# Kernel optimization log

Measured on AMD Instinct MI355X. Metric: run time of the kernel, lower is better.

The kernel has to match this reference:

```python
import jax, jax.numpy as jnp
import numpy as np

H, W = 14, 14
HEAD_DIM = 32
HEADS = 24
HIDDEN = 768
RATE = 0.2
EPS = 1e-5


def _bias_idxs(h, w):
    # map_bias indexing: for flat pair index x over (h*w)^2
    x = jnp.arange(h * h * w * w)
    m, n = x // (h * w), x % (h * w)
    i, j = m // w, m % w
    ip, jp = n // w, n % w
    return (i - ip + h) * (2 * w) + (j - jp + w)


def _layer_norm(x, g, b):
    mu = jnp.mean(x, axis=-1, keepdims=True)
    var = jnp.mean(jnp.square(x - mu), axis=-1, keepdims=True)
    return (x - mu) * jax.lax.rsqrt(var + EPS) * g + b


def setup_inputs() -> dict:
    key = jax.random.key(0)
    ks = jax.random.split(key, 10)
    N, L = 64, H * W
    s = lambda fan_in: 1.0 / np.sqrt(fan_in)
    return {
        "x": jax.random.normal(ks[0], (N, L, HIDDEN), jnp.float32),
        "rel_bias": jax.random.uniform(ks[1], (1, 2 * H * 2 * W), jnp.float32, -0.5, 0.5),
        "wq": jax.random.normal(ks[2], (HEAD_DIM, HEAD_DIM), jnp.float32) * s(HEAD_DIM),
        "wk": jax.random.normal(ks[3], (HEAD_DIM, HEAD_DIM), jnp.float32) * s(HEAD_DIM),
        "wv": jax.random.normal(ks[4], (HEAD_DIM, HEAD_DIM), jnp.float32) * s(HEAD_DIM),
        "w_out": jax.random.normal(ks[5], (HIDDEN, HIDDEN), jnp.float32) * s(HIDDEN),
        "ln1_g": jnp.ones((HIDDEN,), jnp.float32),
        "ln1_b": jnp.zeros((HIDDEN,), jnp.float32),
        "ln2_g": jnp.ones((HIDDEN,), jnp.float32),
        "ln2_b": jnp.zeros((HIDDEN,), jnp.float32),
        "w1": jax.random.normal(ks[6], (4 * HIDDEN, HIDDEN), jnp.float32) * s(HIDDEN),
        "b1": jnp.zeros((4 * HIDDEN,), jnp.float32),
        "w2": jax.random.normal(ks[7], (HIDDEN, 4 * HIDDEN), jnp.float32) * s(4 * HIDDEN),
        "b2": jnp.zeros((HIDDEN,), jnp.float32),
    }


def reference(x, rel_bias, wq, wk, wv, w_out, ln1_g, ln1_b, ln2_g, ln2_b, w1, b1, w2, b2):
    N, L, _ = x.shape

    def attn(m):
        xh = m.reshape(N, L, HEADS, HEAD_DIM)
        # Linear(head_dim, head_dim) shared across heads; torch Linear: y = x @ W^T
        q = jnp.einsum("nlhd,ed->nlhe", xh, wq)
        k = jnp.einsum("nlhd,ed->nlhe", xh, wk)
        v = jnp.einsum("nlhd,ed->nlhe", xh, wv)
        scores = jnp.einsum("nqhd,nkhd->nhqk", q, k)
        bias = rel_bias[0][_bias_idxs(H, W)].reshape(1, 1, L, L)
        a = jax.nn.softmax((scores + bias) / np.sqrt(HEAD_DIM), axis=-1)
        o = jnp.einsum("nhqk,nkhd->nqhd", a, v).reshape(N, L, HIDDEN)
        return o @ w_out.T

    def ffn(m):
        h = jax.nn.gelu(m @ w1.T + b1, approximate=False)
        return h @ w2.T + b2

    # training-mode stochastic depth: deterministic scaling by RATE
    x = (x + attn(_layer_norm(x, ln1_g, ln1_b))) * RATE
    x = (x + ffn(_layer_norm(x, ln2_g, ln2_b))) * RATE
    return x
```

## Files before the change

### kernel.cpp

```cpp
#include <hip/hip_runtime.h>
#include <math.h>

#define NB    64
#define LSEQ  196
#define HID   768
#define NHEAD 24
#define HDIM  32
#define FFN   3072
#define ROWS  (NB * LSEQ)
#define RATE  0.2f
#define LN_EPS 1e-5f

typedef unsigned short bf16_t;
typedef short s16x8 __attribute__((ext_vector_type(8)));
typedef float f32x4 __attribute__((ext_vector_type(4)));

__device__ __forceinline__ unsigned short f2bf(float f) {
    unsigned u = __float_as_uint(f);
    unsigned r = u + 0x7fffu + ((u >> 16) & 1u);
    return (unsigned short)(r >> 16);
}

#define GLOAD_LDS16(g, l)                                                  \
    __builtin_amdgcn_global_load_lds(                                      \
        (const __attribute__((address_space(1))) void*)(g),                \
        (__attribute__((address_space(3))) void*)(l), 16, 0, 0)

#define WOUT4 (HID * HID / 4)
#define W14   (FFN * HID / 4)
__global__ __launch_bounds__(256) void cvt_w_kernel(
    const float* __restrict__ w_out, const float* __restrict__ w1,
    const float* __restrict__ w2, bf16_t* __restrict__ wob,
    bf16_t* __restrict__ w1b, bf16_t* __restrict__ w2b)
{
    int i = blockIdx.x * 256 + threadIdx.x;
    const float* src; bf16_t* dst; int off;
    if (i < WOUT4)            { src = w_out; dst = wob; off = i; }
    else if (i < WOUT4 + W14) { src = w1;    dst = w1b; off = i - WOUT4; }
    else                      { src = w2;    dst = w2b; off = i - WOUT4 - W14; }
    float4 v = ((const float4*)src)[off];
    uint2 p;
    p.x = (unsigned)f2bf(v.x) | ((unsigned)f2bf(v.y) << 16);
    p.y = (unsigned)f2bf(v.z) | ((unsigned)f2bf(v.w) << 16);
    ((uint2*)dst)[off] = p;
}

__global__ __launch_bounds__(256) void ln_kernel(
    const float* __restrict__ x, const float* __restrict__ g,
    const float* __restrict__ b, bf16_t* __restrict__ yv)
{
    int row = blockIdx.x;
    int tid = threadIdx.x;
    const float* xr = x + (size_t)row * HID;
    float v0 = xr[tid], v1 = xr[tid + 256], v2 = xr[tid + 512];
    __shared__ float rs[256], rs2[256];
    rs[tid]  = v0 + v1 + v2;
    rs2[tid] = v0 * v0 + v1 * v1 + v2 * v2;
    __syncthreads();
    for (int off = 128; off > 0; off >>= 1) {
        if (tid < off) { rs[tid] += rs[tid + off]; rs2[tid] += rs2[tid + off]; }
        __syncthreads();
    }
    float mean = rs[0] * (1.0f / HID);
    float var  = rs2[0] * (1.0f / HID) - mean * mean;
    float rstd = rsqrtf(var + LN_EPS);
    bf16_t* yr = yv + (size_t)row * HID;
    yr[tid]       = f2bf((v0 - mean) * rstd * g[tid]       + b[tid]);
    yr[tid + 256] = f2bf((v1 - mean) * rstd * g[tid + 256] + b[tid + 256]);
    yr[tid + 512] = f2bf((v2 - mean) * rstd * g[tid + 512] + b[tid + 512]);
}

#define QKV_T 16
__global__ __launch_bounds__(256) void ln_qkv_mfma_kernel(
    const float* __restrict__ x, const float* __restrict__ g,
    const float* __restrict__ b,
    const float* __restrict__ wq, const float* __restrict__ wk,
    const float* __restrict__ wv,
    bf16_t* __restrict__ q, bf16_t* __restrict__ k, bf16_t* __restrict__ v)
{
    int tid = threadIdx.x;
    int w = tid >> 6, lane = tid & 63;
    int lr = lane & 15, lq = lane >> 4;

    __shared__ __align__(16) bf16_t Xs[QKV_T * 24 * 32];
    __shared__ __align__(16) bf16_t Wqs[32 * 32];
    __shared__ __align__(16) bf16_t Wks[32 * 32];
    __shared__ __align__(16) bf16_t Wvs[32 * 32];

    for (int i = tid; i < 1024; i += 256) {
        Wqs[i] = f2bf(wq[i]);
        Wks[i] = f2bf(wk[i]);
        Wvs[i] = f2bf(wv[i]);
    }

    float4 gv[3], bv[3];
#pragma unroll
    for (int i = 0; i < 3; i++) {
        gv[i] = ((const float4*)g)[lane + i * 64];
        bv[i] = ((const float4*)b)[lane + i * 64];
    }

    for (int j = 0; j < 4; j++) {
        int lt = w * 4 + j;
        size_t row = (size_t)blockIdx.x * QKV_T + lt;
        const float4* xr = (const float4*)(x + row * HID);
        float4 xv[3];
        float s = 0.f, s2 = 0.f;
#pragma unroll
        for (int i = 0; i < 3; i++) {
            xv[i] = xr[lane + i * 64];
            s  += xv[i].x + xv[i].y + xv[i].z + xv[i].w;
            s2 += xv[i].x * xv[i].x + xv[i].y * xv[i].y
                + xv[i].z * xv[i].z + xv[i].w * xv[i].w;
        }
#pragma unroll
        for (int d = 1; d < 64; d <<= 1) {
            s  += __shfl_xor(s, d);
            s2 += __shfl_xor(s2, d);
        }
        float mean = s * (1.0f / HID);
        float rstd = rsqrtf(s2 * (1.0f / HID) - mean * mean + LN_EPS);
#pragma unroll
        for (int i = 0; i < 3; i++) {
            int idx  = (lane + i * 64) * 4;
            int head = idx >> 5, d0 = idx & 31;
            float o0 = (xv[i].x - mean) * rstd * gv[i].x + bv[i].x;
            float o1 = (xv[i].y - mean) * rstd * gv[i].y + bv[i].y;
            float o2 = (xv[i].z - mean) * rstd * gv[i].z + bv[i].z;
            float o3 = (xv[i].w - mean) * rstd * gv[i].w + bv[i].w;
            uint2 p;
            p.x = (unsigned)f2bf(o0) | ((unsigned)f2bf(o1) << 16);
            p.y = (unsigned)f2bf(o2) | ((unsigned)f2bf(o3) << 16);
            *(uint2*)&Xs[(lt * 24 + head) * 32 + d0] = p;
        }
    }
    __syncthreads();

    s16x8 bq[2], bk[2], bvv[2];
    bq[0]  = *(const s16x8*)&Wqs[lr * 32 + lq * 8];
    bq[1]  = *(const s16x8*)&Wqs[(16 + lr) * 32 + lq * 8];
    bk[0]  = *(const s16x8*)&Wks[lr * 32 + lq * 8];
    bk[1]  = *(const s16x8*)&Wks[(16 + lr) * 32 + lq * 8];
    bvv[0] = *(const s16x8*)&Wvs[lr * 32 + lq * 8];
    bvv[1] = *(const s16x8*)&Wvs[(16 + lr) * 32 + lq * 8];

    for (int t = 0; t < 6; t++) {
        int tile = w * 6 + t;
        s16x8 aX = *(const s16x8*)&Xs[(tile * 16 + lr) * 32 + lq * 8];
        f32x4 z = {};
        f32x4 aq0 = __builtin_amdgcn_mfma_f32_16x16x32_bf16(aX, bq[0],  z, 0, 0, 0);
        f32x4 aq1 = __builtin_amdgcn_mfma_f32_16x16x32_bf16(aX, bq[1],  z, 0, 0, 0);
        f32x4 ak0 = __builtin_amdgcn_mfma_f32_16x16x32_bf16(aX, bk[0],  z, 0, 0, 0);
        f32x4 ak1 = __builtin_amdgcn_mfma_f32_16x16x32_bf16(aX, bk[1],  z, 0, 0, 0);
        f32x4 av0 = __builtin_amdgcn_mfma_f32_16x16x32_bf16(aX, bvv[0], z, 0, 0, 0);
        f32x4 av1 = __builtin_amdgcn_mfma_f32_16x16x32_bf16(aX, bvv[1], z, 0, 0, 0);
        int rbase = tile * 16 + lq * 4;
#pragma unroll
        for (int r = 0; r < 4; r++) {
            int xrow = rbase + r;
            int t_loc = xrow / 24, head = xrow - t_loc * 24;
            size_t gb = ((size_t)blockIdx.x * QKV_T + t_loc) * HID + head * 32;
            q[gb + lr]      = f2bf(aq0[r]);
            q[gb + 16 + lr] = f2bf(aq1[r]);
            k[gb + lr]      = f2bf(ak0[r]);
            k[gb + 16 + lr] = f2bf(ak1[r]);
            v[gb + lr]      = f2bf(av0[r]);
            v[gb + 16 + lr] = f2bf(av1[r]);
        }
    }
}

#define VT_S 232
#define P_S  40

__global__ __launch_bounds__(256) void attn_mfma_kernel(
    const bf16_t* __restrict__ q, const bf16_t* __restrict__ k,
    const bf16_t* __restrict__ v, const float* __restrict__ rel_bias,
    bf16_t* __restrict__ o)
{
    int h = blockIdx.x;
    int n = blockIdx.y;
    int tid = threadIdx.x;
    int w = tid >> 6, lane = tid & 63;
    int lr = lane & 15;
    int lq = lane >> 4;

    __shared__ __align__(16) bf16_t Qs[208 * 32];
    __shared__ __align__(16) bf16_t Ks[224 * 32];
    __shared__ __align__(16) bf16_t Vt[32 * VT_S];
    __shared__ float bsh[28 * 28];
    __shared__ __align__(16) bf16_t Ps[4][16 * P_S];

    size_t base = (size_t)n * LSEQ * HID + (size_t)h * HDIM;

    for (int i = tid; i < 224 * 4; i += 256) {
        int r = i >> 2, c = i & 3;
        uint4 kv = make_uint4(0, 0, 0, 0);
        if (r < 196) kv = *(const uint4*)&k[base + (size_t)r * HID + c * 8];
        *(uint4*)&Ks[r * 32 + c * 8] = kv;
        if (r < 208) {
            uint4 qv = make_uint4(0, 0, 0, 0);
            if (r < 196) qv = *(const uint4*)&q[base + (size_t)r * HID + c * 8];
            *(uint4*)&Qs[r * 32 + c * 8] = qv;
        }
    }
    for (int i = tid; i < 196 * 16; i += 256) {
        int key = i >> 4, d2 = (i & 15) * 2;
        unsigned u = *(const unsigned*)&v[base + (size_t)key * HID + d2];
        Vt[d2 * VT_S + key]       = (bf16_t)(u & 0xffffu);
        Vt[(d2 + 1) * VT_S + key] = (bf16_t)(u >> 16);
    }
    for (int i = tid; i < 32 * 32; i += 256) {
        int d = i >> 5, kp = i & 31;
        if (kp < 28) Vt[d * VT_S + 196 + kp] = 0;
    }
    for (int i = tid; i < 784; i += 256) bsh[i] = rel_bias[i];
    __syncthreads();

    const float inv_sqrt_d = 0.17677669529663687f;
    bf16_t* P = Ps[w];

    for (int qt = w; qt < 13; qt += 4) {
        s16x8 aQ = *(const s16x8*)&Qs[(qt * 16 + lr) * 32 + lq * 8];

        int bb[4]; bool qvalid[4];
#pragma unroll
        for (int r = 0; r < 4; r++) {
            int qr = qt * 16 + lq * 4 + r;
            qvalid[r] = qr < LSEQ;
            int qq = qvalid[r] ? qr : 0;
            int qi = qq / 14, qj = qq - 14 * (qq / 14);
            bb[r] = (qi + 14) * 28 + (qj + 14);
        }

        f32x4 sf[14];
#pragma unroll
        for (int kt = 0; kt < 14; kt++) {
            s16x8 bK = *(const s16x8*)&Ks[(kt * 16 + lr) * 32 + lq * 8];
            f32x4 z = {};
            sf[kt] = __builtin_amdgcn_mfma_f32_16x16x32_bf16(aQ, bK, z, 0, 0, 0);
        }
#pragma unroll
        for (int kt = 0; kt < 14; kt++) {
            int key = kt * 16 + lr;
            bool kv = key < LSEQ;
            int kk2 = kv ? key : 0;
            int ip = kk2 / 14, jp = kk2 - 14 * ip;
            int boff = ip * 28 + jp;
#pragma unroll
            for (int r = 0; r < 4; r++) {
                float val = (sf[kt][r] + bsh[bb[r] - boff]) * inv_sqrt_d;
                sf[kt][r] = kv ? val : -1e30f;
            }
        }
        float mx[4];
#pragma unroll
        for (int r = 0; r < 4; r++) {
            float m = sf[0][r];
#pragma unroll
            for (int kt = 1; kt < 14; kt++) m = fmaxf(m, sf[kt][r]);
            mx[r] = m;
        }
#pragma unroll
        for (int d = 1; d < 16; d <<= 1)
#pragma unroll
            for (int r = 0; r < 4; r++)
                mx[r] = fmaxf(mx[r], __shfl_xor(mx[r], d));
        float sum[4] = {0.f, 0.f, 0.f, 0.f};
#pragma unroll
        for (int kt = 0; kt < 14; kt++)
#pragma unroll
            for (int r = 0; r < 4; r++) {
                float p = __expf(sf[kt][r] - mx[r]);
                sf[kt][r] = p;
                sum[r] += p;
            }
#pragma unroll
        for (int d = 1; d < 16; d <<= 1)
#pragma unroll
            for (int r = 0; r < 4; r++)
                sum[r] += __shfl_xor(sum[r], d);

        f32x4 oacc[2] = {};
#pragma unroll
        for (int kc = 0; kc < 7; kc++) {
#pragma unroll
            for (int r = 0; r < 4; r++) {
                P[(lq * 4 + r) * P_S + lr]      = f2bf(sf[2 * kc][r]);
                P[(lq * 4 + r) * P_S + 16 + lr] = f2bf(sf[2 * kc + 1][r]);
            }
            s16x8 aP = *(const s16x8*)&P[lr * P_S + lq * 8];
#pragma unroll
            for (int dt = 0; dt < 2; dt++) {
                s16x8 bV = *(const s16x8*)&Vt[(dt * 16 + lr) * VT_S + kc * 32 + lq * 8];
                oacc[dt] = __builtin_amdgcn_mfma_f32_16x16x32_bf16(aP, bV, oacc[dt], 0, 0, 0);
            }
        }
#pragma unroll
        for (int r = 0; r < 4; r++) {
            if (qvalid[r]) {
                float inv_l = 1.0f / sum[r];
                size_t ob = base + (size_t)(qt * 16 + lq * 4 + r) * HID;
                o[ob + lr]      = f2bf(oacc[0][r] * inv_l);
                o[ob + 16 + lr] = f2bf(oacc[1][r] * inv_l);
            }
        }
    }
}

__device__ __forceinline__ float gelu_fast(float x) {
    float z2 = 1.5957691216f * (x + 0.044715f * x * x * x);
    return x - x * __frcp_rn(__expf(z2) + 1.0f);
}

template <int MODE, bool OBF, int TM>
__global__ __launch_bounds__(256) void gemm_mfma(
    const bf16_t* __restrict__ A, const bf16_t* __restrict__ B,
    void* __restrict__ Cv, int M, int N, int K,
    const float* __restrict__ bias, const float* __restrict__ res, float scale)
{
    constexpr int MT = TM / 32;
    __shared__ __align__(16) bf16_t As[TM * 64];
    __shared__ __align__(16) bf16_t Bs[128 * 64];

    int tid = threadIdx.x;
    int mb = M / TM, nb = N >> 7;
    int gblk = blockIdx.x;
    int full = mb & ~7;
    int gfull = full * nb;
    int m_, n_;
    if (gblk < gfull) {
        int sg = gblk / (8 * nb), u = gblk - sg * (8 * nb);
        m_ = sg * 8 + (u & 7); n_ = u >> 3;
    } else {
        int u = gblk - gfull, rem = mb - full;
        m_ = full + u % rem; n_ = u / rem;
    }
    int bm = m_ * TM, bn = n_ << 7;

    int w    = tid >> 6;
    int lane = tid & 63;
    int wm = (w & 1) * (TM / 2);
    int wn = (w >> 1) * 64;
    int lr = lane & 15;
    int lq = lane >> 4;

    int srowl = lane >> 3;
    int scb   = ((lane & 7) ^ srowl) * 16;
    const char* Ab = (const char*)A;
    const char* Bb = (const char*)B;

    f32x4 acc[MT][4] = {};

    for (int k0 = 0; k0 < K; k0 += 64) {
#pragma unroll
        for (int j = 0; j < TM / 32; j++) {
            int rb = w * (TM / 4) + j * 8;
            GLOAD_LDS16(Ab + ((size_t)(bm + rb + srowl) * K + k0) * 2 + scb, &As[rb * 64]);
        }
#pragma unroll
        for (int j = 0; j < 4; j++) {
            int rb = w * 32 + j * 8;
            GLOAD_LDS16(Bb + ((size_t)(bn + rb + srowl) * K + k0) * 2 + scb, &Bs[rb * 64]);
        }
        __syncthreads();

        int sw = lr & 7;
#pragma unroll
        for (int kc = 0; kc < 2; kc++) {
            int cof = (((kc << 2) | lq) ^ sw) * 8;
            s16x8 af[MT], bf[4];
#pragma unroll
            for (int t = 0; t < MT; t++)
                af[t] = *(const s16x8*)&As[(wm + t * 16 + lr) * 64 + cof];
#pragma unroll
            for (int t = 0; t < 4; t++)
                bf[t] = *(const s16x8*)&Bs[(wn + t * 16 + lr) * 64 + cof];
#pragma unroll
            for (int tm = 0; tm < MT; tm++)
#pragma unroll
                for (int tn = 0; tn < 4; tn++)
                    acc[tm][tn] = __builtin_amdgcn_mfma_f32_16x16x32_bf16(
                        af[tm], bf[tn], acc[tm][tn], 0, 0, 0);
        }
        __syncthreads();
    }

#pragma unroll
    for (int tm = 0; tm < MT; tm++) {
#pragma unroll
        for (int tn = 0; tn < 4; tn++) {
#pragma unroll
            for (int r = 0; r < 4; r++) {
                int mrow = bm + wm + tm * 16 + lq * 4 + r;
                int ncol = bn + wn + tn * 16 + lr;
                float vacc = acc[tm][tn][r];
                if (MODE == 1) {
                    vacc = (res[(size_t)mrow * N + ncol] + vacc) * scale;
                } else if (MODE == 2) {
                    vacc = gelu_fast(vacc + bias[ncol]);
                } else if (MODE == 3) {
                    vacc = (res[(size_t)mrow * N + ncol] + vacc + bias[ncol]) * scale;
                }
                if (OBF) ((bf16_t*)Cv)[(size_t)mrow * N + ncol] = f2bf(vacc);
                else     ((float*)Cv)[(size_t)mrow * N + ncol] = vacc;
            }
        }
    }
}

extern "C" void kernel_launch(void* const* d_in, const int* in_sizes, int n_in,
                              void* d_out, int out_size, void* d_ws, size_t ws_size,
                              hipStream_t stream)
{
    const float* x        = (const float*)d_in[0];
    const float* rel_bias = (const float*)d_in[1];
    const float* wq       = (const float*)d_in[2];
    const float* wk       = (const float*)d_in[3];
    const float* wv       = (const float*)d_in[4];
    const float* w_out    = (const float*)d_in[5];
    const float* ln1_g    = (const float*)d_in[6];
    const float* ln1_b    = (const float*)d_in[7];
    const float* ln2_g    = (const float*)d_in[8];
    const float* ln2_b    = (const float*)d_in[9];
    const float* w1       = (const float*)d_in[10];
    const float* b1       = (const float*)d_in[11];
    const float* w2       = (const float*)d_in[12];
    const float* b2       = (const float*)d_in[13];
    float* out = (float*)d_out;
    float* ws  = (float*)d_ws;

    const size_t SZ = (size_t)ROWS * HID;
    bf16_t* q_bf = (bf16_t*)(ws + SZ);
    bf16_t* k_bf = (bf16_t*)(ws + 2 * SZ);
    bf16_t* v_bf = (bf16_t*)(ws + 3 * SZ);
    bf16_t* o_bf = (bf16_t*)ws;
    bf16_t* y2b  = (bf16_t*)(ws + SZ / 2);
    bf16_t* h    = (bf16_t*)(ws + SZ);
    bf16_t* wob  = (bf16_t*)(ws + 4 * SZ);
    bf16_t* w1b  = wob + (size_t)HID * HID;
    bf16_t* w2b  = w1b + (size_t)FFN * HID;

    cvt_w_kernel<<<(WOUT4 + 2 * W14 + 255) / 256, 256, 0, stream>>>(
        w_out, w1, w2, wob, w1b, w2b);

    ln_qkv_mfma_kernel<<<ROWS / QKV_T, 256, 0, stream>>>(
        x, ln1_g, ln1_b, wq, wk, wv, q_bf, k_bf, v_bf);

    attn_mfma_kernel<<<dim3(NHEAD, NB), 256, 0, stream>>>(q_bf, k_bf, v_bf, rel_bias, o_bf);

    gemm_mfma<1, false, 64><<<(ROWS / 64) * (HID / 128), 256, 0, stream>>>(
        o_bf, wob, out, ROWS, HID, HID, nullptr, x, RATE);

    ln_kernel<<<ROWS, 256, 0, stream>>>(out, ln2_g, ln2_b, y2b);

    gemm_mfma<2, true, 128><<<(ROWS / 128) * (FFN / 128), 256, 0, stream>>>(
        y2b, w1b, h, ROWS, FFN, HID, b1, nullptr, 1.0f);

    gemm_mfma<3, false, 64><<<(ROWS / 64) * (HID / 128), 256, 0, stream>>>(
        h, w2b, out, ROWS, HID, FFN, b2, out, RATE);
}
```

Before: 458.9 us.

## Add triple-buffered 256x128 MFMA GEMM for both FFN matmuls

```diff
diff --git a/kernel.cpp b/kernel.cpp
--- a/kernel.cpp
+++ b/kernel.cpp
@@ -388,6 +388,130 @@
 
 #pragma unroll
     for (int tm = 0; tm < MT; tm++) {
+#pragma unroll
+        for (int tn = 0; tn < 4; tn++) {
+#pragma unroll
+            for (int r = 0; r < 4; r++) {
+                int mrow = bm + wm + tm * 16 + lq * 4 + r;
+                int ncol = bn + wn + tn * 16 + lr;
+                float vacc = acc[tm][tn][r];
+                if (MODE == 1) {
+                    vacc = (res[(size_t)mrow * N + ncol] + vacc) * scale;
+                } else if (MODE == 2) {
+                    vacc = gelu_fast(vacc + bias[ncol]);
+                } else if (MODE == 3) {
+                    vacc = (res[(size_t)mrow * N + ncol] + vacc + bias[ncol]) * scale;
+                }
+                if (OBF) ((bf16_t*)Cv)[(size_t)mrow * N + ncol] = f2bf(vacc);
+                else     ((float*)Cv)[(size_t)mrow * N + ncol] = vacc;
+            }
+        }
+    }
+}
+
+template <int MODE, bool OBF>
+__global__ __launch_bounds__(512, 2) void gemm_pipe(
+    const bf16_t* __restrict__ A, const bf16_t* __restrict__ B,
+    void* __restrict__ Cv, int M, int N, int K,
+    const float* __restrict__ bias, const float* __restrict__ res, float scale)
+{
+    constexpr int BM = 256, BN = 128, BK = 64, NBUF = 3;
+    __shared__ __align__(16) bf16_t As[NBUF][BM * BK];
+    __shared__ __align__(16) bf16_t Bs[NBUF][BN * BK];
+
+    int tid  = threadIdx.x;
+    int w    = tid >> 6;
+    int lane = tid & 63;
+
+    int mb = M / BM, nb = N / BN;
+    int gblk = blockIdx.x;
+    int full = mb & ~7;
+    int gfull = full * nb;
+    int m_, n_;
+    if (gblk < gfull) {
+        int sg = gblk / (8 * nb), u = gblk - sg * (8 * nb);
+        m_ = sg * 8 + (u & 7); n_ = u >> 3;
+    } else {
+        int u = gblk - gfull, rem = mb - full;
+        m_ = full + u % rem; n_ = u / rem;
+    }
+    int bm = m_ * BM, bn = n_ * BN;
+
+    int wm = (w >> 1) * 64;
+    int wn = (w & 1) * 64;
+    int lr = lane & 15;
+    int lq = lane >> 4;
+
+    int srowl = lane >> 3;
+    int scb   = ((lane & 7) ^ srowl) * 16;
+    const char* Ab = (const char*)A;
+    const char* Bb = (const char*)B;
+
+    const int NT = K / BK;
+    f32x4 acc[4][4] = {};
+
+    auto stage = [&](int t, int bi) {
+        int k0 = t * BK;
+#pragma unroll
+        for (int j = 0; j < 4; j++) {
+            int rb = j * 64 + w * 8;
+            GLOAD_LDS16(Ab + ((size_t)(bm + rb + srowl) * K + k0) * 2 + scb,
+                        &As[bi][rb * BK]);
+        }
+#pragma unroll
+        for (int j = 0; j < 2; j++) {
+            int rb = j * 64 + w * 8;
+            GLOAD_LDS16(Bb + ((size_t)(bn + rb + srowl) * K + k0) * 2 + scb,
+                        &Bs[bi][rb * BK]);
+        }
+    };
+
+    auto compute = [&](int bi) {
+        int sw = lr & 7;
+        __builtin_amdgcn_s_setprio(1);
+#pragma unroll
+        for (int kc = 0; kc < 2; kc++) {
+            int cof = (((kc << 2) | lq) ^ sw) * 8;
+            s16x8 af[4], bf[4];
+#pragma unroll
+            for (int t = 0; t < 4; t++)
+                af[t] = *(const s16x8*)&As[bi][(wm + t * 16 + lr) * BK + cof];
+#pragma unroll
+            for (int t = 0; t < 4; t++)
+                bf[t] = *(const s16x8*)&Bs[bi][(wn + t * 16 + lr) * BK + cof];
+#pragma unroll
+            for (int tm = 0; tm < 4; tm++)
+#pragma unroll
+                for (int tn = 0; tn < 4; tn++)
+                    acc[tm][tn] = __builtin_amdgcn_mfma_f32_16x16x32_bf16(
+                        af[tm], bf[tn], acc[tm][tn], 0, 0, 0);
+        }
+        __builtin_amdgcn_s_setprio(0);
+    };
+
+    stage(0, 0);
+    stage(1, 1);
+
+    for (int t = 0; t < NT - 2; t++) {
+        stage(t + 2, (t + 2) % 3);
+        asm volatile("s_waitcnt vmcnt(12)" ::: "memory");
+        __builtin_amdgcn_s_barrier();
+        asm volatile("" ::: "memory");
+        compute(t % 3);
+        asm volatile("" ::: "memory");
+        __builtin_amdgcn_s_barrier();
+    }
+    asm volatile("s_waitcnt vmcnt(6)" ::: "memory");
+    __builtin_amdgcn_s_barrier();
+    asm volatile("" ::: "memory");
+    compute((NT - 2) % 3);
+    asm volatile("s_waitcnt vmcnt(0)" ::: "memory");
+    __builtin_amdgcn_s_barrier();
+    asm volatile("" ::: "memory");
+    compute((NT - 1) % 3);
+
+#pragma unroll
+    for (int tm = 0; tm < 4; tm++) {
 #pragma unroll
         for (int tn = 0; tn < 4; tn++) {
 #pragma unroll
@@ -454,9 +578,9 @@
 
     ln_kernel<<<ROWS, 256, 0, stream>>>(out, ln2_g, ln2_b, y2b);
 
-    gemm_mfma<2, true, 128><<<(ROWS / 128) * (FFN / 128), 256, 0, stream>>>(
+    gemm_pipe<2, true><<<(ROWS / 256) * (FFN / 128), 512, 0, stream>>>(
         y2b, w1b, h, ROWS, FFN, HID, b1, nullptr, 1.0f);
 
-    gemm_mfma<3, false, 64><<<(ROWS / 64) * (HID / 128), 256, 0, stream>>>(
+    gemm_pipe<3, false><<<(ROWS / 256) * (HID / 128), 512, 0, stream>>>(
         h, w2b, out, ROWS, HID, FFN, b2, out, RATE);
 }
```

Measured after the change: 499.1 us. 1.09x slower.

## Double-buffer LDS tiles in MFMA GEMM to overlap loads with compute

Applied to the files above, without the earlier changes.

```diff
diff --git a/kernel.cpp b/kernel.cpp
--- a/kernel.cpp
+++ b/kernel.cpp
@@ -320,8 +320,8 @@
     const float* __restrict__ bias, const float* __restrict__ res, float scale)
 {
     constexpr int MT = TM / 32;
-    __shared__ __align__(16) bf16_t As[TM * 64];
-    __shared__ __align__(16) bf16_t Bs[128 * 64];
+    __shared__ __align__(16) bf16_t As[2][TM * 64];
+    __shared__ __align__(16) bf16_t Bs[2][128 * 64];
 
     int tid = threadIdx.x;
     int mb = M / TM, nb = N >> 7;
@@ -352,19 +352,22 @@
 
     f32x4 acc[MT][4] = {};
 
-    for (int k0 = 0; k0 < K; k0 += 64) {
+    auto stage = [&](int k0, int bi) {
 #pragma unroll
         for (int j = 0; j < TM / 32; j++) {
             int rb = w * (TM / 4) + j * 8;
-            GLOAD_LDS16(Ab + ((size_t)(bm + rb + srowl) * K + k0) * 2 + scb, &As[rb * 64]);
+            GLOAD_LDS16(Ab + ((size_t)(bm + rb + srowl) * K + k0) * 2 + scb,
+                        &As[bi][rb * 64]);
         }
 #pragma unroll
         for (int j = 0; j < 4; j++) {
             int rb = w * 32 + j * 8;
-            GLOAD_LDS16(Bb + ((size_t)(bn + rb + srowl) * K + k0) * 2 + scb, &Bs[rb * 64]);
-        }
-        __syncthreads();
-
+            GLOAD_LDS16(Bb + ((size_t)(bn + rb + srowl) * K + k0) * 2 + scb,
+                        &Bs[bi][rb * 64]);
+        }
+    };
+
+    auto compute = [&](int bi) {
         int sw = lr & 7;
 #pragma unroll
         for (int kc = 0; kc < 2; kc++) {
@@ -372,10 +375,10 @@
             s16x8 af[MT], bf[4];
 #pragma unroll
             for (int t = 0; t < MT; t++)
-                af[t] = *(const s16x8*)&As[(wm + t * 16 + lr) * 64 + cof];
+                af[t] = *(const s16x8*)&As[bi][(wm + t * 16 + lr) * 64 + cof];
 #pragma unroll
             for (int t = 0; t < 4; t++)
-                bf[t] = *(const s16x8*)&Bs[(wn + t * 16 + lr) * 64 + cof];
+                bf[t] = *(const s16x8*)&Bs[bi][(wn + t * 16 + lr) * 64 + cof];
 #pragma unroll
             for (int tm = 0; tm < MT; tm++)
 #pragma unroll
@@ -383,8 +386,22 @@
                     acc[tm][tn] = __builtin_amdgcn_mfma_f32_16x16x32_bf16(
                         af[tm], bf[tn], acc[tm][tn], 0, 0, 0);
         }
-        __syncthreads();
-    }
+    };
+
+    stage(0, 0);
+    asm volatile("s_waitcnt vmcnt(0)" ::: "memory");
+    __builtin_amdgcn_s_barrier();
+
+    const int nt = K >> 6;
+    int cur = 0;
+    for (int t = 0; t < nt - 1; ++t) {
+        stage((t + 1) << 6, cur ^ 1);
+        compute(cur);
+        asm volatile("s_waitcnt vmcnt(0)" ::: "memory");
+        __builtin_amdgcn_s_barrier();
+        cur ^= 1;
+    }
+    compute(cur);
 
 #pragma unroll
     for (int tm = 0; tm < MT; tm++) {
```

After: 453.8 us. About the same (-1.1%).
